# Kernel optimization log

Hardware: AMD Instinct MI355X
Metric: run time of the kernel (lower is better)

## Reference

```python
import jax, jax.numpy as jnp
import numpy as np

B, C, D, H, W = 4, 64, 32, 64, 64
S, NH = 8, 4
HD = C // NH


def setup_inputs() -> dict:
    key = jax.random.key(0)
    ks = jax.random.split(key, 8)
    sc = 0.05
    return {
        "x": jax.random.normal(ks[0], (B, C, D, H, W), jnp.float32),
        "slot_init": jax.random.normal(ks[1], (1, C, S), jnp.float32),
        "slot_proj_w": jax.random.normal(ks[2], (C, C), jnp.float32) * sc,
        "slot_proj_b": jnp.zeros((C,), jnp.float32),
        "ln_g": jnp.ones((C,), jnp.float32),
        "ln_b": jnp.zeros((C,), jnp.float32),
        "in_proj_w": jax.random.normal(ks[3], (3 * C, C), jnp.float32) * sc,
        "in_proj_b": jnp.zeros((3 * C,), jnp.float32),
        "out_proj_w": jax.random.normal(ks[4], (C, C), jnp.float32) * sc,
        "out_proj_b": jnp.zeros((C,), jnp.float32),
        "feat_w": jax.random.normal(ks[5], (C, C), jnp.float32) * sc,
        "feat_b": jnp.zeros((C,), jnp.float32),
        "s2f_w": jax.random.normal(ks[6], (C, C), jnp.float32) * sc,
        "s2f_b": jnp.zeros((C,), jnp.float32),
    }


def _l2norm(v, axis):
    # F.normalize: v / max(||v||, eps)
    n = jnp.sqrt(jnp.sum(v * v, axis=axis, keepdims=True))
    return v / jnp.maximum(n, 1e-12)


def reference(x, slot_init, slot_proj_w, slot_proj_b, ln_g, ln_b,
              in_proj_w, in_proj_b, out_proj_w, out_proj_b,
              feat_w, feat_b, s2f_w, s2f_b):
    b, c, d, h, w = x.shape
    n = d * h * w
    x_flat = x.reshape(b, c, n)                                  # (b,c,N)
    slots = jnp.broadcast_to(slot_init, (b, c, S))               # (b,c,S)

    # ---- slot update: cosine-sim cross attention over N ----
    x_norm = _l2norm(x_flat, 1)
    slots_norm = _l2norm(slots, 1)
    sim = jnp.einsum('bcs,bcn->bsn', slots_norm, x_norm)         # (b,S,N)
    attn = jax.nn.softmax(sim, axis=2)
    updates = jnp.einsum('bcn,bsn->bsc', x_flat, attn)           # (b,S,c)
    slots_t = updates @ slot_proj_w.T + slot_proj_b              # (b,S,c)

    # ---- LayerNorm(channels) then tiny MHSA over S=8 slots ----
    mu = jnp.mean(slots_t, axis=-1, keepdims=True)
    var = jnp.mean((slots_t - mu) ** 2, axis=-1, keepdims=True)
    sn = (slots_t - mu) / jnp.sqrt(var + 1e-5) * ln_g + ln_b     # (b,S,c)

    qkv = sn @ in_proj_w.T + in_proj_b                           # (b,S,3c)
    q, k, v = jnp.split(qkv, 3, axis=-1)
    def heads(t):
        return t.reshape(b, S, NH, HD).transpose(0, 2, 1, 3)     # (b,H,S,hd)
    q, k, v = heads(q), heads(k), heads(v)
    scores = jnp.einsum('bhqd,bhkd->bhqk', q, k) / jnp.sqrt(jnp.float32(HD))
    a = jax.nn.softmax(scores, axis=-1)
    o = jnp.einsum('bhqk,bhkd->bhqd', a, v).transpose(0, 2, 1, 3).reshape(b, S, c)
    o = o @ out_proj_w.T + out_proj_b
    slots_t = slots_t + o                                        # (b,S,c)

    # ---- feature broadcast: 1x1x1 conv + slot->feature attention ----
    feat_flat = jnp.einsum('oc,bcn->bon', feat_w, x_flat) + feat_b[None, :, None]
    slots_feat = slots_t @ s2f_w.T + s2f_b                       # (b,S,c)
    sim2 = jnp.einsum('bsc,bcn->bsn', slots_feat, feat_flat)
    attn2 = jax.nn.softmax(sim2, axis=1)                         # softmax over slots
    out = jnp.einsum('bsc,bsn->bcn', slots_t, attn2)             # (b,c,N)
    return out.reshape(b, c, d, h, w) + x
```

## Files before the change

### kernel.cpp

```cpp
#include <hip/hip_runtime.h>
#include <hip/hip_bf16.h>

#define BB   4
#define CC   64
#define SS   8
#define NN   (32*64*64)
#define NH_  4
#define HD_  16
#define TN   256
#define BPB  128

__global__ __launch_bounds__(256) void k_slots_attn(
    const float* __restrict__ x, const float* __restrict__ slot_init,
    float* __restrict__ U_part, float* __restrict__ sume_part)
{
    __shared__ float xt[CC * TN];
    __shared__ float et[SS * TN];
    __shared__ float snT[SS * CC];
    __shared__ float snorm[SS];

    const int tid = threadIdx.x;
    const int b   = blockIdx.x / BPB;
    const int blk = blockIdx.x % BPB;

    if (tid < SS) {
        float ss = 0.f;
        for (int c = 0; c < CC; ++c) { float v = slot_init[c*SS + tid]; ss += v*v; }
        snorm[tid] = fmaxf(sqrtf(ss), 1e-12f);
    }
    __syncthreads();
    if (tid < CC) {
        for (int s = 0; s < SS; ++s) snT[s*CC + tid] = slot_init[tid*SS + s] / snorm[s];
    }
    __syncthreads();

    const int s_own = tid >> 5;
    const int c0    = tid & 31;
    const int c1    = c0 + 32;
    float acc0 = 0.f, acc1 = 0.f, accS = 0.f;

    const float* xb = x + (size_t)b * CC * NN;
    const int ntiles = NN / TN;
    const int wrow = tid >> 6;
    const int j    = tid & 63;

    for (int t = blk; t < ntiles; t += BPB) {
        const int n0 = t * TN;

        #pragma unroll
        for (int k = 0; k < 16; ++k) {
            const int c = k*4 + wrow;
            float4 v = *(const float4*)(xb + (size_t)c * NN + n0 + j*4);
            const int slot = c*64 + (j ^ (c & 7));
            *(float4*)(&xt[slot*4]) = v;
        }
        __syncthreads();

        {
            float ss = 0.f;
            float a[SS];
            #pragma unroll
            for (int s = 0; s < SS; ++s) a[s] = 0.f;
            #pragma unroll
            for (int c4 = 0; c4 < 16; ++c4) {
                float xv[4];
                #pragma unroll
                for (int jj = 0; jj < 4; ++jj) {
                    const int c = c4*4 + jj;
                    xv[jj] = xt[c*TN + (tid ^ ((c & 7) << 2))];
                    ss += xv[jj] * xv[jj];
                }
                #pragma unroll
                for (int s = 0; s < SS; ++s) {
                    float4 g4 = *(const float4*)(&snT[s*CC + c4*4]);
                    a[s] += g4.x*xv[0] + g4.y*xv[1] + g4.z*xv[2] + g4.w*xv[3];
                }
            }
            const float invn = 1.f / fmaxf(sqrtf(ss), 1e-12f);
            #pragma unroll
            for (int s = 0; s < SS; ++s) et[s*TN + tid] = __expf(a[s] * invn);
        }
        __syncthreads();

        #pragma unroll 4
        for (int np4 = 0; np4 < TN/4; ++np4) {
            const float4 e4 = *(const float4*)(&et[s_own*TN + np4*4]);
            const float4 xa = *(const float4*)(&xt[(c0*64 + (np4 ^ (c0 & 7))) * 4]);
            const float4 xc = *(const float4*)(&xt[(c1*64 + (np4 ^ (c1 & 7))) * 4]);
            acc0 += e4.x*xa.x + e4.y*xa.y + e4.z*xa.z + e4.w*xa.w;
            acc1 += e4.x*xc.x + e4.y*xc.y + e4.z*xc.z + e4.w*xc.w;
            accS += e4.x + e4.y + e4.z + e4.w;
        }
        __syncthreads();
    }

    size_t base = (((size_t)b * BPB + blk) * SS + s_own) * CC;
    U_part[base + c0] = acc0;
    U_part[base + c1] = acc1;
    if (c0 == 0)
        sume_part[((size_t)b * BPB + blk) * SS + s_own] = accS;
}

__global__ __launch_bounds__(256) void k_precomp(
    const float* __restrict__ s2fw, const float* __restrict__ s2fb,
    const float* __restrict__ fw, const float* __restrict__ fb,
    float* __restrict__ M, float* __restrict__ g0v,
    float* __restrict__ hv, float* __restrict__ h0)
{
    const int tid = threadIdx.x;
    if (blockIdx.x < 16) {
        const int cp = blockIdx.x*4 + (tid >> 6);
        const int c  = tid & 63;
        float acc = 0.f;
        #pragma unroll 8
        for (int o = 0; o < CC; ++o)
            acc += s2fw[o*CC + cp] * fw[o*CC + c];
        M[cp*CC + c] = acc;
    } else {
        if (tid < 64) {
            float acc = 0.f;
            #pragma unroll 8
            for (int o = 0; o < CC; ++o) acc += s2fb[o] * fw[o*CC + tid];
            g0v[tid] = acc;
        } else if (tid < 128) {
            const int cp = tid - 64;
            float acc = 0.f;
            #pragma unroll 8
            for (int o = 0; o < CC; ++o) acc += s2fw[o*CC + cp] * fb[o];
            hv[cp] = acc;
        } else if (tid == 128) {
            float acc = 0.f;
            for (int o = 0; o < CC; ++o) acc += s2fb[o] * fb[o];
            *h0 = acc;
        }
    }
}

__global__ __launch_bounds__(256) void k_reduce2(
    const float* __restrict__ U_part, const float* __restrict__ sume_part,
    float* __restrict__ upd_g)
{
    __shared__ float part[4][64];
    __shared__ float lbuf[128];
    __shared__ float Lsh;
    const int tid = threadIdx.x;
    const int b = blockIdx.x >> 3, s = blockIdx.x & 7;
    const int c = tid & 63, kc = tid >> 6;

    float lv = 0.f;
    if (tid < 128) lv = sume_part[(size_t)(b*BPB + tid)*SS + s];

    float acc = 0.f;
    const float* base = U_part + ((size_t)(b*BPB + kc*32)*SS + s)*CC + c;
    #pragma unroll 8
    for (int k = 0; k < 32; ++k)
        acc += base[(size_t)k * SS * CC];
    part[kc][c] = acc;
    if (tid < 128) lbuf[tid] = lv;
    __syncthreads();

    if (tid < 64) {
        float v = lbuf[tid] + lbuf[tid + 64];
        v += __shfl_xor(v, 1); v += __shfl_xor(v, 2); v += __shfl_xor(v, 4);
        v += __shfl_xor(v, 8); v += __shfl_xor(v, 16); v += __shfl_xor(v, 32);
        if (tid == 0) Lsh = v;
    }
    __syncthreads();

    if (tid < 64) {
        float u = part[0][c] + part[1][c] + part[2][c] + part[3][c];
        upd_g[((size_t)b*SS + s)*CC + c] = u / Lsh;
    }
}

__global__ __launch_bounds__(256) void k_slots_small(
    const float* __restrict__ upd_g,
    const float* __restrict__ spw, const float* __restrict__ spb,
    const float* __restrict__ lng, const float* __restrict__ lnb,
    const float* __restrict__ ipw, const float* __restrict__ ipb,
    const float* __restrict__ opw, const float* __restrict__ opb,
    const float* __restrict__ M, const float* __restrict__ g0v,
    const float* __restrict__ hv, const float* __restrict__ h0,
    float* __restrict__ st_out, float* __restrict__ g_out, float* __restrict__ h_out)
{
    __shared__ float upd[SS*CC];
    __shared__ float st [SS*CC];
    __shared__ float snb[SS*CC];
    __shared__ float qkv[SS*3*CC];
    __shared__ float ot [SS*CC];

    const int tid  = threadIdx.x;
    const int b    = blockIdx.x;
    const int c    = tid & 63;
    const int quad = tid >> 6;
    const int r0 = quad*2, r1 = r0 + 1;
    float wreg[CC];

    #pragma unroll
    for (int i = 0; i < 16; ++i)
        *(float4*)&wreg[i*4] = *(const float4*)(spw + c*CC + i*4);
    upd[r0*CC + c] = upd_g[(b*SS + r0)*CC + c];
    upd[r1*CC + c] = upd_g[(b*SS + r1)*CC + c];
    __syncthreads();

    {
        const float bias = spb[c];
        float a0 = bias, a1 = bias;
        #pragma unroll
        for (int i = 0; i < 16; ++i) {
            float4 u0 = *(const float4*)&upd[r0*CC + i*4];
            float4 u1 = *(const float4*)&upd[r1*CC + i*4];
            a0 += u0.x*wreg[i*4+0] + u0.y*wreg[i*4+1] + u0.z*wreg[i*4+2] + u0.w*wreg[i*4+3];
            a1 += u1.x*wreg[i*4+0] + u1.y*wreg[i*4+1] + u1.z*wreg[i*4+2] + u1.w*wreg[i*4+3];
        }
        st[r0*CC + c] = a0;
        st[r1*CC + c] = a1;
    }
    __syncthreads();

    {
        const int row = tid >> 5, l = tid & 31;
        float v0 = st[row*CC + l], v1 = st[row*CC + l + 32];
        float sum = v0 + v1;
        sum += __shfl_xor(sum, 1); sum += __shfl_xor(sum, 2); sum += __shfl_xor(sum, 4);
        sum += __shfl_xor(sum, 8); sum += __shfl_xor(sum, 16);
        const float mu = sum * (1.f/64.f);
        const float d0 = v0 - mu, d1 = v1 - mu;
        float vs = d0*d0 + d1*d1;
        vs += __shfl_xor(vs, 1); vs += __shfl_xor(vs, 2); vs += __shfl_xor(vs, 4);
        vs += __shfl_xor(vs, 8); vs += __shfl_xor(vs, 16);
        const float rstd = rsqrtf(vs * (1.f/64.f) + 1e-5f);
        snb[row*CC + l]      = d0 * rstd * lng[l]      + lnb[l];
        snb[row*CC + l + 32] = d1 * rstd * lng[l + 32] + lnb[l + 32];
    }
    __syncthreads();

    for (int m = 0; m < 3; ++m) {
        #pragma unroll
        for (int i = 0; i < 16; ++i)
            *(float4*)&wreg[i*4] = *(const float4*)(ipw + (size_t)(m*CC + c)*CC + i*4);
        const float bias = ipb[m*CC + c];
        float a0 = bias, a1 = bias;
        #pragma unroll
        for (int i = 0; i < 16; ++i) {
            float4 u0 = *(const float4*)&snb[r0*CC + i*4];
            float4 u1 = *(const float4*)&snb[r1*CC + i*4];
            a0 += u0.x*wreg[i*4+0] + u0.y*wreg[i*4+1] + u0.z*wreg[i*4+2] + u0.w*wreg[i*4+3];
            a1 += u1.x*wreg[i*4+0] + u1.y*wreg[i*4+1] + u1.z*wreg[i*4+2] + u1.w*wreg[i*4+3];
        }
        qkv[r0*3*CC + m*CC + c] = a0;
        qkv[r1*3*CC + m*CC + c] = a1;
    }
    __syncthreads();

    if (tid < NH_*SS) {
        const int h = tid >> 3, q = tid & 7;
        float qreg[HD_];
        #pragma unroll
        for (int i = 0; i < 4; ++i)
            *(float4*)&qreg[i*4] = *(const float4*)&qkv[q*3*CC + h*HD_ + i*4];
        float srow[SS];
        float mx = -1e30f;
        #pragma unroll
        for (int k = 0; k < SS; ++k) {
            float acc = 0.f;
            #pragma unroll
            for (int d = 0; d < HD_; ++d)
                acc += qreg[d] * qkv[k*3*CC + CC + h*HD_ + d];
            srow[k] = acc * 0.25f;
            mx = fmaxf(mx, srow[k]);
        }
        float l = 0.f;
        #pragma unroll
        for (int k = 0; k < SS; ++k) { srow[k] = __expf(srow[k] - mx); l += srow[k]; }
        const float inv = 1.f / l;
        float oreg[HD_];
        #pragma unroll
        for (int d = 0; d < HD_; ++d) oreg[d] = 0.f;
        #pragma unroll
        for (int k = 0; k < SS; ++k) {
            #pragma unroll
            for (int d = 0; d < HD_; ++d)
                oreg[d] += srow[k] * qkv[k*3*CC + 2*CC + h*HD_ + d];
        }
        #pragma unroll
        for (int d = 0; d < HD_; ++d)
            ot[q*CC + h*HD_ + d] = oreg[d] * inv;
    }
    __syncthreads();

    #pragma unroll
    for (int i = 0; i < 16; ++i)
        *(float4*)&wreg[i*4] = *(const float4*)(opw + c*CC + i*4);
    {
        const float bias = opb[c];
        float a0 = bias, a1 = bias;
        #pragma unroll
        for (int i = 0; i < 16; ++i) {
            float4 u0 = *(const float4*)&ot[r0*CC + i*4];
            float4 u1 = *(const float4*)&ot[r1*CC + i*4];
            a0 += u0.x*wreg[i*4+0] + u0.y*wreg[i*4+1] + u0.z*wreg[i*4+2] + u0.w*wreg[i*4+3];
            a1 += u1.x*wreg[i*4+0] + u1.y*wreg[i*4+1] + u1.z*wreg[i*4+2] + u1.w*wreg[i*4+3];
        }
        st[r0*CC + c] += a0;
        st[r1*CC + c] += a1;
    }
    __syncthreads();

    #pragma unroll 8
    for (int cp = 0; cp < CC; ++cp) wreg[cp] = M[cp*CC + c];
    {
        const float g0 = g0v[c];
        float a0 = g0, a1 = g0;
        #pragma unroll
        for (int i = 0; i < 16; ++i) {
            float4 s0 = *(const float4*)&st[r0*CC + i*4];
            float4 s1 = *(const float4*)&st[r1*CC + i*4];
            a0 += s0.x*wreg[i*4+0] + s0.y*wreg[i*4+1] + s0.z*wreg[i*4+2] + s0.w*wreg[i*4+3];
            a1 += s1.x*wreg[i*4+0] + s1.y*wreg[i*4+1] + s1.z*wreg[i*4+2] + s1.w*wreg[i*4+3];
        }
        g_out[(b*SS + r0)*CC + c] = a0;
        g_out[(b*SS + r1)*CC + c] = a1;
        st_out[(b*SS + r0)*CC + c] = st[r0*CC + c];
        st_out[(b*SS + r1)*CC + c] = st[r1*CC + c];
    }
    {
        const int row = tid >> 5, l = tid & 31;
        float pv = st[row*CC + l]*hv[l] + st[row*CC + l + 32]*hv[l + 32];
        pv += __shfl_xor(pv, 1); pv += __shfl_xor(pv, 2); pv += __shfl_xor(pv, 4);
        pv += __shfl_xor(pv, 8); pv += __shfl_xor(pv, 16);
        if (l == 0) h_out[b*SS + row] = pv + *h0;
    }
}

__global__ __launch_bounds__(256) void k_feat(
    const float* __restrict__ x,
    const float* __restrict__ st_g, const float* __restrict__ g_g,
    const float* __restrict__ h_g,
    float* __restrict__ out)
{
    __shared__ float stS[SS*CC];
    __shared__ float gS [SS*CC];
    __shared__ float hS [SS];

    const int tid = threadIdx.x;
    const int b  = blockIdx.x >> 9;
    const int n  = ((blockIdx.x & 511) << 8) + tid;

    for (int i = tid; i < SS*CC; i += 256) {
        stS[i] = st_g[b*SS*CC + i];
        gS[i]  = g_g [b*SS*CC + i];
    }
    if (tid < SS) hS[tid] = h_g[b*SS + tid];
    __syncthreads();

    const float* xb = x + (size_t)b * CC * NN + n;
    float xc[CC];
    #pragma unroll
    for (int c = 0; c < CC; ++c) xc[c] = xb[(size_t)c * NN];

    float a[SS];
    #pragma unroll
    for (int s = 0; s < SS; ++s) a[s] = hS[s];
    #pragma unroll
    for (int c4 = 0; c4 < CC/4; ++c4) {
        #pragma unroll
        for (int s = 0; s < SS; ++s) {
            float4 g4 = *(const float4*)(&gS[s*CC + c4*4]);
            a[s] += g4.x*xc[c4*4+0] + g4.y*xc[c4*4+1]
                  + g4.z*xc[c4*4+2] + g4.w*xc[c4*4+3];
        }
    }

    float m = a[0];
    #pragma unroll
    for (int s = 1; s < SS; ++s) m = fmaxf(m, a[s]);
    float l = 0.f;
    #pragma unroll
    for (int s = 0; s < SS; ++s) { a[s] = __expf(a[s] - m); l += a[s]; }
    const float inv = 1.f / l;

    float* ob = out + (size_t)b * CC * NN + n;
    #pragma unroll
    for (int c4 = 0; c4 < CC/4; ++c4) {
        float o0 = 0.f, o1 = 0.f, o2 = 0.f, o3 = 0.f;
        #pragma unroll
        for (int s = 0; s < SS; ++s) {
            float4 s4 = *(const float4*)(&stS[s*CC + c4*4]);
            o0 += s4.x * a[s]; o1 += s4.y * a[s];
            o2 += s4.z * a[s]; o3 += s4.w * a[s];
        }
        ob[(size_t)(c4*4+0) * NN] = o0 * inv + xc[c4*4+0];
        ob[(size_t)(c4*4+1) * NN] = o1 * inv + xc[c4*4+1];
        ob[(size_t)(c4*4+2) * NN] = o2 * inv + xc[c4*4+2];
        ob[(size_t)(c4*4+3) * NN] = o3 * inv + xc[c4*4+3];
    }
}

extern "C" void kernel_launch(void* const* d_in, const int* in_sizes, int n_in,
                              void* d_out, int out_size, void* d_ws, size_t ws_size,
                              hipStream_t stream) {
    const float* x         = (const float*)d_in[0];
    const float* slot_init = (const float*)d_in[1];
    const float* spw       = (const float*)d_in[2];
    const float* spb       = (const float*)d_in[3];
    const float* lng       = (const float*)d_in[4];
    const float* lnb       = (const float*)d_in[5];
    const float* ipw       = (const float*)d_in[6];
    const float* ipb       = (const float*)d_in[7];
    const float* opw       = (const float*)d_in[8];
    const float* opb       = (const float*)d_in[9];
    const float* fw        = (const float*)d_in[10];
    const float* fb        = (const float*)d_in[11];
    const float* s2fw      = (const float*)d_in[12];
    const float* s2fb      = (const float*)d_in[13];
    float* out = (float*)d_out;

    float* w         = (float*)d_ws;
    float* U_part    = w;
    float* sume_part = w + 262144;
    float* upd_g     = w + 266240;
    float* Mm        = w + 268288;
    float* g0v       = w + 272384;
    float* hv        = w + 272448;
    float* h0        = w + 272512;
    float* st_out    = w + 272576;
    float* g_out     = w + 274624;
    float* h_out     = w + 276672;

    k_precomp<<<17, 256, 0, stream>>>(s2fw, s2fb, fw, fb, Mm, g0v, hv, h0);
    k_slots_attn<<<BB * BPB, 256, 0, stream>>>(x, slot_init, U_part, sume_part);
    k_reduce2<<<BB * SS, 256, 0, stream>>>(U_part, sume_part, upd_g);
    k_slots_small<<<BB, 256, 0, stream>>>(upd_g, spw, spb, lng, lnb,
                                          ipw, ipb, opw, opb, Mm, g0v, hv, h0,
                                          st_out, g_out, h_out);
    k_feat<<<BB * (NN/256), 256, 0, stream>>>(x, st_out, g_out, h_out, out);
}
```

Baseline: 139.8 us.

## Store slot-attention tiles as fp16 in LDS and double tile width to 512 threads

The slot-attention kernel now converts x to half precision when staging it into shared memory and keeps the exp weights in half as well. This halves LDS footprint and bandwidth, which allows a 512-wide tile with 512 threads per block and one channel per thread in the accumulation phase. The cost is extra conversion instructions and reduced precision for x and the softmax weights, which could push the result outside tolerance. The load pattern and swizzle are redone to match the 8-half vector layout.

Result: slower. 176.8 us (+26.4%).

```diff
diff --git a/kernel.cpp b/kernel.cpp
--- a/kernel.cpp
+++ b/kernel.cpp
@@ -1,5 +1,6 @@
 #include <hip/hip_runtime.h>
 #include <hip/hip_bf16.h>
+#include <hip/hip_fp16.h>
 
 #define BB   4
 #define CC   64
@@ -7,17 +8,17 @@
 #define NN   (32*64*64)
 #define NH_  4
 #define HD_  16
-#define TN   256
+#define TN   512
 #define BPB  128
 
-__global__ __launch_bounds__(256) void k_slots_attn(
+__global__ __launch_bounds__(512, 4) void k_slots_attn(
     const float* __restrict__ x, const float* __restrict__ slot_init,
     float* __restrict__ U_part, float* __restrict__ sume_part)
 {
-    __shared__ float xt[CC * TN];
-    __shared__ float et[SS * TN];
-    __shared__ float snT[SS * CC];
-    __shared__ float snorm[SS];
+    __shared__ __half xt[CC * TN];
+    __shared__ __half et[SS * TN];
+    __shared__ float  snT[SS * CC];
+    __shared__ float  snorm[SS];
 
     const int tid = threadIdx.x;
     const int b   = blockIdx.x / BPB;
@@ -34,29 +35,37 @@
     }
     __syncthreads();
 
-    const int s_own = tid >> 5;
-    const int c0    = tid & 31;
-    const int c1    = c0 + 32;
-    float acc0 = 0.f, acc1 = 0.f, accS = 0.f;
+    const int s_own = tid >> 6;
+    const int c_own = tid & 63;
+    float acc0 = 0.f, accS = 0.f;
 
     const float* xb = x + (size_t)b * CC * NN;
+    const int crow = tid >> 3;
+    const int jg   = tid & 7;
     const int ntiles = NN / TN;
-    const int wrow = tid >> 6;
-    const int j    = tid & 63;
 
     for (int t = blk; t < ntiles; t += BPB) {
         const int n0 = t * TN;
 
-        #pragma unroll
-        for (int k = 0; k < 16; ++k) {
-            const int c = k*4 + wrow;
-            float4 v = *(const float4*)(xb + (size_t)c * NN + n0 + j*4);
-            const int slot = c*64 + (j ^ (c & 7));
-            *(float4*)(&xt[slot*4]) = v;
+        {
+            const float* src = xb + (size_t)crow * NN + n0 + jg*64;
+            #pragma unroll
+            for (int w = 0; w < 8; ++w) {
+                float4 va = *(const float4*)(src + w*8);
+                float4 vb = *(const float4*)(src + w*8 + 4);
+                union { __half2 h2[4]; float4 f4; } u;
+                u.h2[0] = __floats2half2_rn(va.x, va.y);
+                u.h2[1] = __floats2half2_rn(va.z, va.w);
+                u.h2[2] = __floats2half2_rn(vb.x, vb.y);
+                u.h2[3] = __floats2half2_rn(vb.z, vb.w);
+                const int slot = jg*8 + (w ^ (crow & 7));
+                *(float4*)&xt[crow*TN + slot*8] = u.f4;
+            }
         }
         __syncthreads();
 
         {
+            const int qb = tid >> 3, lo = tid & 7;
             float ss = 0.f;
             float a[SS];
             #pragma unroll
@@ -67,7 +76,7 @@
                 #pragma unroll
                 for (int jj = 0; jj < 4; ++jj) {
                     const int c = c4*4 + jj;
-                    xv[jj] = xt[c*TN + (tid ^ ((c & 7) << 2))];
+                    xv[jj] = __half2float(xt[c*TN + ((qb ^ (c & 7)) << 3) + lo]);
                     ss += xv[jj] * xv[jj];
                 }
                 #pragma unroll
@@ -78,26 +87,36 @@
             }
             const float invn = 1.f / fmaxf(sqrtf(ss), 1e-12f);
             #pragma unroll
-            for (int s = 0; s < SS; ++s) et[s*TN + tid] = __expf(a[s] * invn);
+            for (int s = 0; s < SS; ++s)
+                et[s*TN + tid] = __float2half(__expf(a[s] * invn));
         }
         __syncthreads();
 
-        #pragma unroll 4
-        for (int np4 = 0; np4 < TN/4; ++np4) {
-            const float4 e4 = *(const float4*)(&et[s_own*TN + np4*4]);
-            const float4 xa = *(const float4*)(&xt[(c0*64 + (np4 ^ (c0 & 7))) * 4]);
-            const float4 xc = *(const float4*)(&xt[(c1*64 + (np4 ^ (c1 & 7))) * 4]);
-            acc0 += e4.x*xa.x + e4.y*xa.y + e4.z*xa.z + e4.w*xa.w;
-            acc1 += e4.x*xc.x + e4.y*xc.y + e4.z*xc.z + e4.w*xc.w;
-            accS += e4.x + e4.y + e4.z + e4.w;
+        {
+            const __half* xrow = &xt[c_own*TN];
+            const __half* erow = &et[s_own*TN];
+            const int cs = c_own & 7;
+            #pragma unroll 4
+            for (int j = 0; j < TN/8; ++j) {
+                float4 eraw = *(const float4*)&erow[j*8];
+                float4 xraw = *(const float4*)&xrow[(j ^ cs)*8];
+                const __half2* eh = (const __half2*)&eraw;
+                const __half2* xh = (const __half2*)&xraw;
+                #pragma unroll
+                for (int k = 0; k < 4; ++k) {
+                    float2 ef = __half22float2(eh[k]);
+                    float2 xf = __half22float2(xh[k]);
+                    acc0 += ef.x*xf.x + ef.y*xf.y;
+                    accS += ef.x + ef.y;
+                }
+            }
         }
         __syncthreads();
     }
 
     size_t base = (((size_t)b * BPB + blk) * SS + s_own) * CC;
-    U_part[base + c0] = acc0;
-    U_part[base + c1] = acc1;
-    if (c0 == 0)
+    U_part[base + c_own] = acc0;
+    if (c_own == 0)
         sume_part[((size_t)b * BPB + blk) * SS + s_own] = accS;
 }
 
@@ -429,7 +448,7 @@
     float* h_out     = w + 276672;
 
     k_precomp<<<17, 256, 0, stream>>>(s2fw, s2fb, fw, fb, Mm, g0v, hv, h0);
-    k_slots_attn<<<BB * BPB, 256, 0, stream>>>(x, slot_init, U_part, sume_part);
+    k_slots_attn<<<BB * BPB, 512, 0, stream>>>(x, slot_init, U_part, sume_part);
     k_reduce2<<<BB * SS, 256, 0, stream>>>(U_part, sume_part, upd_g);
     k_slots_small<<<BB, 256, 0, stream>>>(upd_g, spw, spb, lng, lnb,
                                           ipw, ipb, opw, opb, Mm, g0v, hv, h0,
```

## Use bf16 MFMA for slot-update reduction with bf16 LDS tiles and more blocks

Applied to the files above, without the earlier changes.

Stores each x tile and the exp-weight tile in LDS as bf16 and computes the slot-weighted sum over N with 16x16x32 bf16 MFMA instructions instead of scalar FMAs. The per-slot exp sums are now accumulated in registers during the exp phase. Blocks per batch rise from 128 to 192, with a fallback to 128 when the workspace is too small. The goal is to cut LDS footprint and ALU time in the first pass over x, at the cost of bf16 rounding in the accumulation and a larger partial-sum reduction.

Result: slower. 144.1 us (+3.0%).

```diff
diff --git a/kernel.cpp b/kernel.cpp
--- a/kernel.cpp
+++ b/kernel.cpp
@@ -8,20 +8,40 @@
 #define NH_  4
 #define HD_  16
 #define TN   256
-#define BPB  128
+
+typedef __attribute__((ext_vector_type(8))) short bf16x8;
+typedef __attribute__((ext_vector_type(4))) float f32x4;
+
+__device__ __forceinline__ float b2f(unsigned short h) {
+    union { unsigned u; float f; } v; v.u = ((unsigned)h) << 16; return v.f;
+}
+__device__ __forceinline__ unsigned short f2b(float f) {
+    union { float f; unsigned u; } v; v.f = f;
+    unsigned r = v.u + 0x7FFFu + ((v.u >> 16) & 1u);
+    return (unsigned short)(r >> 16);
+}
+__device__ __forceinline__ unsigned bfpack(float a, float b) {
+    union { float f; unsigned u; } x, y; x.f = a; y.f = b;
+    unsigned ra = (x.u + 0x7FFFu + ((x.u >> 16) & 1u)) >> 16;
+    unsigned rb = (y.u + 0x7FFFu + ((y.u >> 16) & 1u)) & 0xFFFF0000u;
+    return ra | rb;
+}
 
 __global__ __launch_bounds__(256) void k_slots_attn(
     const float* __restrict__ x, const float* __restrict__ slot_init,
-    float* __restrict__ U_part, float* __restrict__ sume_part)
+    float* __restrict__ U_part, float* __restrict__ sume_part, int bpb)
 {
-    __shared__ float xt[CC * TN];
-    __shared__ float et[SS * TN];
+    __shared__ short xt[CC * TN];
+    __shared__ short et[16 * TN];
     __shared__ float snT[SS * CC];
     __shared__ float snorm[SS];
+    __shared__ float red[SS * 256];
 
     const int tid = threadIdx.x;
-    const int b   = blockIdx.x / BPB;
-    const int blk = blockIdx.x % BPB;
+    const int b   = blockIdx.x / bpb;
+    const int blk = blockIdx.x % bpb;
+
+    *(int4*)&et[8*TN + tid*8] = make_int4(0, 0, 0, 0);
 
     if (tid < SS) {
         float ss = 0.f;
@@ -34,29 +54,39 @@
     }
     __syncthreads();
 
-    const int s_own = tid >> 5;
-    const int c0    = tid & 31;
-    const int c1    = c0 + 32;
-    float acc0 = 0.f, acc1 = 0.f, accS = 0.f;
+    const int lane = tid & 63, wv = tid >> 6;
+    const int cS = tid >> 2, nq = tid & 3;
+    f32x4 accU = {0.f, 0.f, 0.f, 0.f};
+    float accS[SS];
+    #pragma unroll
+    for (int s = 0; s < SS; ++s) accS[s] = 0.f;
 
     const float* xb = x + (size_t)b * CC * NN;
     const int ntiles = NN / TN;
-    const int wrow = tid >> 6;
-    const int j    = tid & 63;
-
-    for (int t = blk; t < ntiles; t += BPB) {
+
+    for (int t = blk; t < ntiles; t += bpb) {
         const int n0 = t * TN;
 
-        #pragma unroll
-        for (int k = 0; k < 16; ++k) {
-            const int c = k*4 + wrow;
-            float4 v = *(const float4*)(xb + (size_t)c * NN + n0 + j*4);
-            const int slot = c*64 + (j ^ (c & 7));
-            *(float4*)(&xt[slot*4]) = v;
+        {
+            const float* srcrow = xb + (size_t)cS * NN + n0;
+            #pragma unroll
+            for (int i = 0; i < 8; ++i) {
+                const int n = nq*8 + i*32;
+                float4 va = *(const float4*)(srcrow + n);
+                float4 vb = *(const float4*)(srcrow + n + 4);
+                int4 o;
+                o.x = (int)bfpack(va.x, va.y);
+                o.y = (int)bfpack(va.z, va.w);
+                o.z = (int)bfpack(vb.x, vb.y);
+                o.w = (int)bfpack(vb.z, vb.w);
+                const int slot = (nq + i*4) ^ (cS & 7);
+                *(int4*)&xt[cS*TN + (slot << 3)] = o;
+            }
         }
         __syncthreads();
 
         {
+            const int nq3 = tid >> 3, n7 = tid & 7;
             float ss = 0.f;
             float a[SS];
             #pragma unroll
@@ -65,40 +95,65 @@
             for (int c4 = 0; c4 < 16; ++c4) {
                 float xv[4];
                 #pragma unroll
-                for (int jj = 0; jj < 4; ++jj) {
-                    const int c = c4*4 + jj;
-                    xv[jj] = xt[c*TN + (tid ^ ((c & 7) << 2))];
-                    ss += xv[jj] * xv[jj];
+                for (int j = 0; j < 4; ++j) {
+                    const int c = c4*4 + j;
+                    unsigned short h = (unsigned short)xt[c*TN + (((nq3 ^ (c & 7)) << 3) | n7)];
+                    xv[j] = b2f(h);
+                    ss += xv[j] * xv[j];
                 }
                 #pragma unroll
                 for (int s = 0; s < SS; ++s) {
-                    float4 g4 = *(const float4*)(&snT[s*CC + c4*4]);
+                    const float4 g4 = *(const float4*)&snT[s*CC + c4*4];
                     a[s] += g4.x*xv[0] + g4.y*xv[1] + g4.z*xv[2] + g4.w*xv[3];
                 }
             }
             const float invn = 1.f / fmaxf(sqrtf(ss), 1e-12f);
             #pragma unroll
-            for (int s = 0; s < SS; ++s) et[s*TN + tid] = __expf(a[s] * invn);
+            for (int s = 0; s < SS; ++s) {
+                float e = __expf(a[s] * invn);
+                accS[s] += e;
+                et[s*TN + (((nq3 ^ s) << 3) | n7)] = (short)f2b(e);
+            }
         }
         __syncthreads();
 
-        #pragma unroll 4
-        for (int np4 = 0; np4 < TN/4; ++np4) {
-            const float4 e4 = *(const float4*)(&et[s_own*TN + np4*4]);
-            const float4 xa = *(const float4*)(&xt[(c0*64 + (np4 ^ (c0 & 7))) * 4]);
-            const float4 xc = *(const float4*)(&xt[(c1*64 + (np4 ^ (c1 & 7))) * 4]);
-            acc0 += e4.x*xa.x + e4.y*xa.y + e4.z*xa.z + e4.w*xa.w;
-            acc1 += e4.x*xc.x + e4.y*xc.y + e4.z*xc.z + e4.w*xc.w;
-            accS += e4.x + e4.y + e4.z + e4.w;
+        {
+            const int ca = (wv << 4) + (lane & 15);
+            const int rb = lane & 15;
+            const int p  = lane >> 4;
+            #pragma unroll
+            for (int k = 0; k < TN/32; ++k) {
+                const int sa = ((((k << 2) + p) ^ (lane & 7)) << 3);
+                bf16x8 af = *(const bf16x8*)&xt[ca*TN + sa];
+                bf16x8 bfr = *(const bf16x8*)&et[rb*TN + sa];
+                accU = __builtin_amdgcn_mfma_f32_16x16x32_bf16(af, bfr, accU, 0, 0, 0);
+            }
         }
         __syncthreads();
     }
 
-    size_t base = (((size_t)b * BPB + blk) * SS + s_own) * CC;
-    U_part[base + c0] = acc0;
-    U_part[base + c1] = acc1;
-    if (c0 == 0)
-        sume_part[((size_t)b * BPB + blk) * SS + s_own] = accS;
+    {
+        const size_t base = ((size_t)(b*bpb + blk) * SS) * CC;
+        if ((lane & 15) < SS) {
+            const int s  = lane & 15;
+            const int c0 = (wv << 4) + ((lane >> 4) << 2);
+            #pragma unroll
+            for (int r = 0; r < 4; ++r)
+                U_part[base + s*CC + c0 + r] = accU[r];
+        }
+    }
+    #pragma unroll
+    for (int s = 0; s < SS; ++s) red[s*256 + tid] = accS[s];
+    __syncthreads();
+    {
+        const int s = tid >> 5, j = tid & 31;
+        float v = 0.f;
+        #pragma unroll
+        for (int k = 0; k < 8; ++k) v += red[s*256 + j*8 + k];
+        v += __shfl_xor(v, 1); v += __shfl_xor(v, 2); v += __shfl_xor(v, 4);
+        v += __shfl_xor(v, 8); v += __shfl_xor(v, 16);
+        if (j == 0) sume_part[(size_t)(b*bpb + blk)*SS + s] = v;
+    }
 }
 
 __global__ __launch_bounds__(256) void k_precomp(
@@ -138,27 +193,27 @@
 
 __global__ __launch_bounds__(256) void k_reduce2(
     const float* __restrict__ U_part, const float* __restrict__ sume_part,
-    float* __restrict__ upd_g)
+    float* __restrict__ upd_g, int bpb)
 {
     __shared__ float part[4][64];
-    __shared__ float lbuf[128];
+    __shared__ float lbuf[256];
     __shared__ float Lsh;
     const int tid = threadIdx.x;
     const int b = blockIdx.x >> 3, s = blockIdx.x & 7;
     const int c = tid & 63, kc = tid >> 6;
-
-    float lv = 0.f;
-    if (tid < 128) lv = sume_part[(size_t)(b*BPB + tid)*SS + s];
+    const int cnt = bpb >> 2;
+
+    lbuf[tid] = (tid < bpb) ? sume_part[(size_t)(b*bpb + tid)*SS + s] : 0.f;
 
     float acc = 0.f;
-    const float* base = U_part + ((size_t)(b*BPB + kc*32)*SS + s)*CC + c;
-    #pragma unroll 8
-    for (int k = 0; k < 32; ++k)
+    const float* base = U_part + ((size_t)(b*bpb + kc*cnt)*SS + s)*CC + c;
+    for (int k = 0; k < cnt; ++k)
         acc += base[(size_t)k * SS * CC];
     part[kc][c] = acc;
-    if (tid < 128) lbuf[tid] = lv;
-    __syncthreads();
-
+    __syncthreads();
+
+    if (tid < 128) lbuf[tid] += lbuf[tid + 128];
+    __syncthreads();
     if (tid < 64) {
         float v = lbuf[tid] + lbuf[tid + 64];
         v += __shfl_xor(v, 1); v += __shfl_xor(v, 2); v += __shfl_xor(v, 4);
@@ -416,21 +471,28 @@
     const float* s2fb      = (const float*)d_in[13];
     float* out = (float*)d_out;
 
+    int bpb = 192;
+    {
+        size_t need = ((size_t)BB*bpb*SS*CC + (size_t)BB*bpb*SS
+                       + 2048 + 4096 + 64 + 64 + 64 + 2048 + 2048 + 32) * sizeof(float);
+        if (need > ws_size) bpb = 128;
+    }
+
     float* w         = (float*)d_ws;
     float* U_part    = w;
-    float* sume_part = w + 262144;
-    float* upd_g     = w + 266240;
-    float* Mm        = w + 268288;
-    float* g0v       = w + 272384;
-    float* hv        = w + 272448;
-    float* h0        = w + 272512;
-    float* st_out    = w + 272576;
-    float* g_out     = w + 274624;
-    float* h_out     = w + 276672;
+    float* sume_part = U_part + (size_t)BB*bpb*SS*CC;
+    float* upd_g     = sume_part + (size_t)BB*bpb*SS;
+    float* Mm        = upd_g + 2048;
+    float* g0v       = Mm + 4096;
+    float* hv        = g0v + 64;
+    float* h0        = hv + 64;
+    float* st_out    = h0 + 64;
+    float* g_out     = st_out + 2048;
+    float* h_out     = g_out + 2048;
 
     k_precomp<<<17, 256, 0, stream>>>(s2fw, s2fb, fw, fb, Mm, g0v, hv, h0);
-    k_slots_attn<<<BB * BPB, 256, 0, stream>>>(x, slot_init, U_part, sume_part);
-    k_reduce2<<<BB * SS, 256, 0, stream>>>(U_part, sume_part, upd_g);
+    k_slots_attn<<<BB * bpb, 256, 0, stream>>>(x, slot_init, U_part, sume_part, bpb);
+    k_reduce2<<<BB * SS, 256, 0, stream>>>(U_part, sume_part, upd_g, bpb);
     k_slots_small<<<BB, 256, 0, stream>>>(upd_g, spw, spb, lng, lnb,
                                           ipw, ipb, opw, opb, Mm, g0v, hv, h0,
                                           st_out, g_out, h_out);
```
